# Performance work log

Measured on AMD Instinct MI355X. Metric: run time of the kernel, lower is better.

Reference implementation:

```python
import jax, jax.numpy as jnp
import numpy as np

DELTA_INF = 1e10  # delta appended for the last sample, as in the torch code
EPS = 1e-10


def setup_inputs() -> dict:
    key = jax.random.key(0)
    k1, k2, k3 = jax.random.split(key, 3)
    N, S = 131072, 192
    ray_samples = jax.random.normal(k1, (N, S, 3), dtype=jnp.float32)
    densities = jax.random.normal(k2, (N, S, 1), dtype=jnp.float32)
    rgb = jax.random.uniform(k3, (N, S, 3), dtype=jnp.float32)
    background_color = jnp.ones((3,), dtype=jnp.float32)
    return {"ray_samples": ray_samples, "densities": densities, "rgb": rgb,
            "background_color": background_color}


def _render_weights(ray_samples, densities):
    # delta_i = ||x_{i+1} - x_i||, last delta = 1e10  -> [N, S, 1]
    diff = ray_samples[..., 1:, :] - ray_samples[..., :-1, :]
    delta = jnp.linalg.norm(diff, axis=-1, keepdims=True)
    delta = jnp.concatenate(
        [delta, jnp.full_like(delta[..., -1:, :], DELTA_INF)], axis=-2)
    alpha = 1.0 - jnp.exp(-jax.nn.relu(densities) * delta)
    # transmittance T_i = prod_{j<i} (1 - alpha_j + eps), exclusive cumprod
    trans = jnp.cumprod(
        jnp.concatenate(
            [jnp.ones_like(alpha[..., :1, :]), 1.0 - alpha + EPS], axis=-2),
        axis=-2)[..., :-1, :]
    weights = alpha * trans  # [N, S, 1]
    return weights


def reference(ray_samples, densities, rgb, background_color):
    weights = _render_weights(ray_samples, densities)
    rendered_rgb = jnp.sum(weights * rgb, axis=-2)           # [N, 3]
    accumulated_alpha = jnp.sum(weights, axis=-2)            # [N, 1]
    # composite with background: img + bg * (1 - acc)
    rendered_rgb = rendered_rgb + background_color * (1.0 - accumulated_alpha)
    return rendered_rgb, accumulated_alpha[..., 0], weights
```

## Files before the change

### kernel.cpp

```cpp
#include <hip/hip_runtime.h>

constexpr int NRAYS = 131072;
constexpr float DELTA_INF_F = 1e10f;
constexpr float EPS_F = 1e-10f;

__global__ __launch_bounds__(256) void nerf_render_kernel(
    const float4* __restrict__ rsF4,
    const float4* __restrict__ denF4,
    const float4* __restrict__ rgbF4,
    const float* __restrict__ bg,
    float* __restrict__ out_rgb,
    float* __restrict__ out_acc,
    float4* __restrict__ out_wF4)
{
    __shared__ float pos[4][576];
    __shared__ float den[4][192];
    __shared__ float wbuf[4][192];

    const int lane = threadIdx.x & 63;
    const int w    = threadIdx.x >> 6;
    const int ray  = (blockIdx.x << 2) + w;

    const float4* rg = rgbF4 + (size_t)ray * 144;
    float4 c0 = rg[lane];
    float4 c1 = rg[lane + 64];
    float4 c2 = make_float4(0.f, 0.f, 0.f, 0.f);
    if (lane < 16) c2 = rg[lane + 128];

    const float4* rp = rsF4 + (size_t)ray * 144;
    float4 p0 = rp[lane];
    float4 p1 = rp[lane + 64];
    float4 p2 = make_float4(0.f, 0.f, 0.f, 0.f);
    if (lane < 16) p2 = rp[lane + 128];

    float4 dd = make_float4(0.f, 0.f, 0.f, 0.f);
    if (lane < 48) dd = denF4[(size_t)ray * 48 + lane];

    float4* pl = (float4*)&pos[w][0];
    pl[lane]      = p0;
    pl[lane + 64] = p1;
    if (lane < 16) pl[lane + 128] = p2;
    if (lane < 48) ((float4*)&den[w][0])[lane] = dd;

    __syncthreads();

    const int pb = 9 * lane;
    float q0x = pos[w][pb+0], q0y = pos[w][pb+1], q0z = pos[w][pb+2];
    float q1x = pos[w][pb+3], q1y = pos[w][pb+4], q1z = pos[w][pb+5];
    float q2x = pos[w][pb+6], q2y = pos[w][pb+7], q2z = pos[w][pb+8];

    float dx = q1x - q0x, dy = q1y - q0y, dz = q1z - q0z;
    float d0 = sqrtf(dx*dx + dy*dy + dz*dz);
    dx = q2x - q1x; dy = q2y - q1y; dz = q2z - q1z;
    float d1 = sqrtf(dx*dx + dy*dy + dz*dz);
    float d2 = DELTA_INF_F;
    if (lane < 63) {
        float nx = pos[w][pb+9], ny = pos[w][pb+10], nz = pos[w][pb+11];
        dx = nx - q2x; dy = ny - q2y; dz = nz - q2z;
        d2 = sqrtf(dx*dx + dy*dy + dz*dz);
    }

    float s0 = den[w][3*lane+0], s1 = den[w][3*lane+1], s2 = den[w][3*lane+2];
    float e0 = expf(-fmaxf(s0, 0.f) * d0);
    float e1 = expf(-fmaxf(s1, 0.f) * d1);
    float e2 = expf(-fmaxf(s2, 0.f) * d2);

    float a0 = 1.f - e0, a1 = 1.f - e1, a2 = 1.f - e2;
    float t0 = (1.f - a0) + EPS_F;
    float t1 = (1.f - a1) + EPS_F;
    float t2 = (1.f - a2) + EPS_F;

    float incl = t0 * t1 * t2;
#pragma unroll
    for (int off = 1; off < 64; off <<= 1) {
        float t = __shfl_up(incl, off);
        if (lane >= off) incl *= t;
    }
    float pref = __shfl_up(incl, 1);
    if (lane == 0) pref = 1.f;

    float w0 = a0 * pref;
    float w1 = a1 * pref * t0;
    float w2 = a2 * pref * t0 * t1;
    float acc = w0 + w1 + w2;

    wbuf[w][3*lane+0] = w0;
    wbuf[w][3*lane+1] = w1;
    wbuf[w][3*lane+2] = w2;

    __syncthreads();

    if (lane < 48)
        out_wF4[(size_t)ray * 48 + lane] = ((const float4*)&wbuf[w][0])[lane];

    float a_0 = 0.f, a_1 = 0.f, a_2 = 0.f;
    {
        const float* cv0 = &c0.x;
        const float* cv1 = &c1.x;
        const float* cv2 = &c2.x;
#pragma unroll
        for (int j = 0; j < 4; ++j) {
            float m0 = cv0[j] * wbuf[w][lane + (lane + j) / 3];
            if ((j + 0) % 3 == 0) a_0 += m0; else if ((j + 0) % 3 == 1) a_1 += m0; else a_2 += m0;
            float m1 = cv1[j] * wbuf[w][lane + 85 + (lane + j + 1) / 3];
            if ((j + 1) % 3 == 0) a_0 += m1; else if ((j + 1) % 3 == 1) a_1 += m1; else a_2 += m1;
            if (lane < 16) {
                float m2 = cv2[j] * wbuf[w][lane + 170 + (lane + j + 2) / 3];
                if ((j + 2) % 3 == 0) a_0 += m2; else if ((j + 2) % 3 == 1) a_1 += m2; else a_2 += m2;
            }
        }
    }
    const int b = lane % 3;
    float cr = (b == 0) ? a_0 : ((b == 1) ? a_2 : a_1);
    float cg = (b == 0) ? a_1 : ((b == 1) ? a_0 : a_2);
    float cb = (b == 0) ? a_2 : ((b == 1) ? a_1 : a_0);

#pragma unroll
    for (int off = 32; off >= 1; off >>= 1) {
        cr  += __shfl_xor(cr, off);
        cg  += __shfl_xor(cg, off);
        cb  += __shfl_xor(cb, off);
        acc += __shfl_xor(acc, off);
    }

    if (lane == 0) {
        float om = 1.f - acc;
        out_rgb[(size_t)ray*3 + 0] = cr + bg[0] * om;
        out_rgb[(size_t)ray*3 + 1] = cg + bg[1] * om;
        out_rgb[(size_t)ray*3 + 2] = cb + bg[2] * om;
        out_acc[ray] = acc;
    }
}

extern "C" void kernel_launch(void* const* d_in, const int* in_sizes, int n_in,
                              void* d_out, int out_size, void* d_ws, size_t ws_size,
                              hipStream_t stream) {
    const float4* rsF4  = (const float4*)d_in[0];
    const float4* denF4 = (const float4*)d_in[1];
    const float4* rgbF4 = (const float4*)d_in[2];
    const float*  bg    = (const float*)d_in[3];

    float* o = (float*)d_out;
    float*  out_rgb = o;
    float*  out_acc = o + (size_t)NRAYS * 3;
    float4* out_wF4 = (float4*)(o + (size_t)NRAYS * 4);

    dim3 grid(NRAYS / 4), block(256);
    hipLaunchKernelGGL(nerf_render_kernel, grid, block, 0, stream,
                       rsF4, denF4, rgbF4, bg, out_rgb, out_acc, out_wF4);
}
```

Before: 159.9 us.

## Use persistent waves with register prefetch and a 4-sample-per-lane layout without LDS

Each lane now owns four consecutive samples and loads them straight from global memory as three float4s, so the shared-memory staging and block barriers are gone. The neighbour position comes from a wave shuffle. The grid shrinks to a fixed 2048 blocks, and each wave loops over many rays while prefetching the next ray's data into registers, so loads overlap with compute. The change also switches to the fast __expf intrinsic. The lane-strided float4 loads (stride of 3 float4s) may coalesce less well, and only 48 of 64 lanes do work.

```diff
diff --git a/kernel.cpp b/kernel.cpp
--- a/kernel.cpp
+++ b/kernel.cpp
@@ -3,6 +3,10 @@
 constexpr int NRAYS = 131072;
 constexpr float DELTA_INF_F = 1e10f;
 constexpr float EPS_F = 1e-10f;
+constexpr int GRID  = 2048;
+constexpr int BLOCK = 256;
+constexpr int WAVES = GRID * (BLOCK / 64);
+constexpr int ITERS = NRAYS / WAVES;
 
 __global__ __launch_bounds__(256) void nerf_render_kernel(
     const float4* __restrict__ rsF4,
@@ -13,122 +17,104 @@
     float* __restrict__ out_acc,
     float4* __restrict__ out_wF4)
 {
-    __shared__ float pos[4][576];
-    __shared__ float den[4][192];
-    __shared__ float wbuf[4][192];
+    const int lane = threadIdx.x & 63;
+    const int gw   = (int)((blockIdx.x * BLOCK + threadIdx.x) >> 6);
+    const bool act = lane < 48;
+    const float bg0 = bg[0], bg1 = bg[1], bg2 = bg[2];
+    const float4 Z = make_float4(0.f, 0.f, 0.f, 0.f);
 
-    const int lane = threadIdx.x & 63;
-    const int w    = threadIdx.x >> 6;
-    const int ray  = (blockIdx.x << 2) + w;
-
-    const float4* rg = rgbF4 + (size_t)ray * 144;
-    float4 c0 = rg[lane];
-    float4 c1 = rg[lane + 64];
-    float4 c2 = make_float4(0.f, 0.f, 0.f, 0.f);
-    if (lane < 16) c2 = rg[lane + 128];
-
-    const float4* rp = rsF4 + (size_t)ray * 144;
-    float4 p0 = rp[lane];
-    float4 p1 = rp[lane + 64];
-    float4 p2 = make_float4(0.f, 0.f, 0.f, 0.f);
-    if (lane < 16) p2 = rp[lane + 128];
-
-    float4 dd = make_float4(0.f, 0.f, 0.f, 0.f);
-    if (lane < 48) dd = denF4[(size_t)ray * 48 + lane];
-
-    float4* pl = (float4*)&pos[w][0];
-    pl[lane]      = p0;
-    pl[lane + 64] = p1;
-    if (lane < 16) pl[lane + 128] = p2;
-    if (lane < 48) ((float4*)&den[w][0])[lane] = dd;
-
-    __syncthreads();
-
-    const int pb = 9 * lane;
-    float q0x = pos[w][pb+0], q0y = pos[w][pb+1], q0z = pos[w][pb+2];
-    float q1x = pos[w][pb+3], q1y = pos[w][pb+4], q1z = pos[w][pb+5];
-    float q2x = pos[w][pb+6], q2y = pos[w][pb+7], q2z = pos[w][pb+8];
-
-    float dx = q1x - q0x, dy = q1y - q0y, dz = q1z - q0z;
-    float d0 = sqrtf(dx*dx + dy*dy + dz*dz);
-    dx = q2x - q1x; dy = q2y - q1y; dz = q2z - q1z;
-    float d1 = sqrtf(dx*dx + dy*dy + dz*dz);
-    float d2 = DELTA_INF_F;
-    if (lane < 63) {
-        float nx = pos[w][pb+9], ny = pos[w][pb+10], nz = pos[w][pb+11];
-        dx = nx - q2x; dy = ny - q2y; dz = nz - q2z;
-        d2 = sqrtf(dx*dx + dy*dy + dz*dz);
+    int ray = gw;
+    float4 P0 = Z, P1 = Z, P2 = Z, D = Z, C0 = Z, C1 = Z, C2 = Z;
+    if (act) {
+        const float4* rp = rsF4 + (size_t)ray * 144 + 3 * lane;
+        P0 = rp[0]; P1 = rp[1]; P2 = rp[2];
+        D = denF4[(size_t)ray * 48 + lane];
+        const float4* rc = rgbF4 + (size_t)ray * 144 + 3 * lane;
+        C0 = rc[0]; C1 = rc[1]; C2 = rc[2];
     }
 
-    float s0 = den[w][3*lane+0], s1 = den[w][3*lane+1], s2 = den[w][3*lane+2];
-    float e0 = expf(-fmaxf(s0, 0.f) * d0);
-    float e1 = expf(-fmaxf(s1, 0.f) * d1);
-    float e2 = expf(-fmaxf(s2, 0.f) * d2);
+#pragma unroll 2
+    for (int it = 0; it < ITERS; ++it) {
+        int nray = ray + WAVES;
+        float4 nP0 = Z, nP1 = Z, nP2 = Z, nD = Z, nC0 = Z, nC1 = Z, nC2 = Z;
+        if (act && (it + 1 < ITERS)) {
+            const float4* rp = rsF4 + (size_t)nray * 144 + 3 * lane;
+            nP0 = rp[0]; nP1 = rp[1]; nP2 = rp[2];
+            nD = denF4[(size_t)nray * 48 + lane];
+            const float4* rc = rgbF4 + (size_t)nray * 144 + 3 * lane;
+            nC0 = rc[0]; nC1 = rc[1]; nC2 = rc[2];
+        }
 
-    float a0 = 1.f - e0, a1 = 1.f - e1, a2 = 1.f - e2;
-    float t0 = (1.f - a0) + EPS_F;
-    float t1 = (1.f - a1) + EPS_F;
-    float t2 = (1.f - a2) + EPS_F;
+        float x0 = P0.x, y0 = P0.y, z0 = P0.z;
+        float x1 = P0.w, y1 = P1.x, z1 = P1.y;
+        float x2 = P1.z, y2 = P1.w, z2 = P2.x;
+        float x3 = P2.y, y3 = P2.z, z3 = P2.w;
 
-    float incl = t0 * t1 * t2;
+        float nx = __shfl_down(x0, 1);
+        float ny = __shfl_down(y0, 1);
+        float nz = __shfl_down(z0, 1);
+
+        float dx = x1 - x0, dy = y1 - y0, dz = z1 - z0;
+        float d0 = sqrtf(dx * dx + dy * dy + dz * dz);
+        dx = x2 - x1; dy = y2 - y1; dz = z2 - z1;
+        float d1 = sqrtf(dx * dx + dy * dy + dz * dz);
+        dx = x3 - x2; dy = y3 - y2; dz = z3 - z2;
+        float d2 = sqrtf(dx * dx + dy * dy + dz * dz);
+        dx = nx - x3; dy = ny - y3; dz = nz - z3;
+        float d3 = (lane == 47) ? DELTA_INF_F : sqrtf(dx * dx + dy * dy + dz * dz);
+
+        float e0 = __expf(-fmaxf(D.x, 0.f) * d0);
+        float e1 = __expf(-fmaxf(D.y, 0.f) * d1);
+        float e2 = __expf(-fmaxf(D.z, 0.f) * d2);
+        float e3 = __expf(-fmaxf(D.w, 0.f) * d3);
+        float a0 = 1.f - e0, a1 = 1.f - e1, a2 = 1.f - e2, a3 = 1.f - e3;
+        float t0 = (1.f - a0) + EPS_F;
+        float t1 = (1.f - a1) + EPS_F;
+        float t2 = (1.f - a2) + EPS_F;
+        float t3 = (1.f - a3) + EPS_F;
+
+        float t01 = t0 * t1;
+        float t012 = t01 * t2;
+        float incl = t012 * t3;
 #pragma unroll
-    for (int off = 1; off < 64; off <<= 1) {
-        float t = __shfl_up(incl, off);
-        if (lane >= off) incl *= t;
-    }
-    float pref = __shfl_up(incl, 1);
-    if (lane == 0) pref = 1.f;
+        for (int off = 1; off < 64; off <<= 1) {
+            float t = __shfl_up(incl, off);
+            if (lane >= off) incl *= t;
+        }
+        float pref = __shfl_up(incl, 1);
+        if (lane == 0) pref = 1.f;
 
-    float w0 = a0 * pref;
-    float w1 = a1 * pref * t0;
-    float w2 = a2 * pref * t0 * t1;
-    float acc = w0 + w1 + w2;
+        float w0 = a0 * pref;
+        float w1 = a1 * pref * t0;
+        float w2 = a2 * pref * t01;
+        float w3 = a3 * pref * t012;
+        float acc = w0 + w1 + w2 + w3;
 
-    wbuf[w][3*lane+0] = w0;
-    wbuf[w][3*lane+1] = w1;
-    wbuf[w][3*lane+2] = w2;
+        if (act)
+            out_wF4[(size_t)ray * 48 + lane] = make_float4(w0, w1, w2, w3);
 
-    __syncthreads();
-
-    if (lane < 48)
-        out_wF4[(size_t)ray * 48 + lane] = ((const float4*)&wbuf[w][0])[lane];
-
-    float a_0 = 0.f, a_1 = 0.f, a_2 = 0.f;
-    {
-        const float* cv0 = &c0.x;
-        const float* cv1 = &c1.x;
-        const float* cv2 = &c2.x;
-#pragma unroll
-        for (int j = 0; j < 4; ++j) {
-            float m0 = cv0[j] * wbuf[w][lane + (lane + j) / 3];
-            if ((j + 0) % 3 == 0) a_0 += m0; else if ((j + 0) % 3 == 1) a_1 += m0; else a_2 += m0;
-            float m1 = cv1[j] * wbuf[w][lane + 85 + (lane + j + 1) / 3];
-            if ((j + 1) % 3 == 0) a_0 += m1; else if ((j + 1) % 3 == 1) a_1 += m1; else a_2 += m1;
-            if (lane < 16) {
-                float m2 = cv2[j] * wbuf[w][lane + 170 + (lane + j + 2) / 3];
-                if ((j + 2) % 3 == 0) a_0 += m2; else if ((j + 2) % 3 == 1) a_1 += m2; else a_2 += m2;
-            }
-        }
-    }
-    const int b = lane % 3;
-    float cr = (b == 0) ? a_0 : ((b == 1) ? a_2 : a_1);
-    float cg = (b == 0) ? a_1 : ((b == 1) ? a_0 : a_2);
-    float cb = (b == 0) ? a_2 : ((b == 1) ? a_1 : a_0);
+        float cr = w0 * C0.x + w1 * C0.w + w2 * C1.z + w3 * C2.y;
+        float cg = w0 * C0.y + w1 * C1.x + w2 * C1.w + w3 * C2.z;
+        float cb = w0 * C0.z + w1 * C1.y + w2 * C2.x + w3 * C2.w;
 
 #pragma unroll
-    for (int off = 32; off >= 1; off >>= 1) {
-        cr  += __shfl_xor(cr, off);
-        cg  += __shfl_xor(cg, off);
-        cb  += __shfl_xor(cb, off);
-        acc += __shfl_xor(acc, off);
-    }
+        for (int off = 32; off >= 1; off >>= 1) {
+            cr  += __shfl_xor(cr, off);
+            cg  += __shfl_xor(cg, off);
+            cb  += __shfl_xor(cb, off);
+            acc += __shfl_xor(acc, off);
+        }
 
-    if (lane == 0) {
-        float om = 1.f - acc;
-        out_rgb[(size_t)ray*3 + 0] = cr + bg[0] * om;
-        out_rgb[(size_t)ray*3 + 1] = cg + bg[1] * om;
-        out_rgb[(size_t)ray*3 + 2] = cb + bg[2] * om;
-        out_acc[ray] = acc;
+        if (lane == 0) {
+            float om = 1.f - acc;
+            out_rgb[(size_t)ray * 3 + 0] = cr + bg0 * om;
+            out_rgb[(size_t)ray * 3 + 1] = cg + bg1 * om;
+            out_rgb[(size_t)ray * 3 + 2] = cb + bg2 * om;
+            out_acc[ray] = acc;
+        }
+
+        P0 = nP0; P1 = nP1; P2 = nP2; D = nD; C0 = nC0; C1 = nC1; C2 = nC2;
+        ray = nray;
     }
 }
 
@@ -145,7 +131,7 @@
     float*  out_acc = o + (size_t)NRAYS * 3;
     float4* out_wF4 = (float4*)(o + (size_t)NRAYS * 4);
 
-    dim3 grid(NRAYS / 4), block(256);
+    dim3 grid(GRID), block(BLOCK);
     hipLaunchKernelGGL(nerf_render_kernel, grid, block, 0, stream,
                        rsF4, denF4, rgbF4, bg, out_rgb, out_acc, out_wF4);
 }
```

Result: slower. 170.2 us (+6.4%).
